# Performance work log

Hardware: AMD Instinct MI355X
Metric: run time of the kernel (lower is better)

The kernel has to match this reference:

```python
import jax, jax.numpy as jnp
import numpy as np

B, N, D_IN, D_OUT, H = 2, 2048, 1024, 1024, 16
HEAD_DIM = D_OUT // H


def setup_inputs() -> dict:
    key = jax.random.key(0)
    ks = jax.random.split(key, 8)
    s = 0.02
    return {
        "x": jax.random.normal(ks[0], (B, N, D_IN), dtype=jnp.float32),
        "Wq": jax.random.normal(ks[1], (D_IN, D_OUT), dtype=jnp.float32) * s,
        "Wk": jax.random.normal(ks[2], (D_IN, D_OUT), dtype=jnp.float32) * s,
        "Wv": jax.random.normal(ks[3], (D_IN, D_OUT), dtype=jnp.float32) * s,
        "Wo": jax.random.normal(ks[4], (D_OUT, D_OUT), dtype=jnp.float32) * s,
        "bo": jnp.zeros((D_OUT,), dtype=jnp.float32),
        "w": jax.random.uniform(ks[5], (H,), dtype=jnp.float32),
        "v": jax.random.uniform(ks[6], (H,), dtype=jnp.float32),
    }


def reference(x, Wq, Wk, Wv, Wo, bo, w, v):
    b, n, _ = x.shape
    h = w.shape[0]
    hd = Wq.shape[1] // h

    # QKV projections -> [b, h, n, hd]
    def proj(W):
        return (x @ W).reshape(b, n, h, hd).transpose(0, 2, 1, 3)

    q, k, val = proj(Wq), proj(Wk), proj(Wv)

    # relative-distance decay R_hat: [h, n, n]
    pos = jnp.arange(n)
    R = jnp.abs(pos[:, None] - pos[None, :]).astype(x.dtype)  # [n, n]
    wv = w[:, None, None]
    vv = v[:, None, None]
    R_hat = (1.0 + jnp.exp(vv)) / (1.0 + jnp.exp(vv - wv * R))  # [h, n, n]

    # ReLU(QK^T) * R_hat, causal mask, scaled softmax
    scores = jax.nn.relu(jnp.einsum("bhqd,bhkd->bhqk", q, k)) * R_hat[None]
    causal = jnp.triu(jnp.ones((n, n), dtype=bool), k=1)
    scores = jnp.where(causal[None, None], -jnp.inf, scores)
    attn = jax.nn.softmax(scores / np.sqrt(hd).astype(x.dtype), axis=-1)

    ctx = jnp.einsum("bhqk,bhkd->bhqd", attn, val)
    ctx = ctx.transpose(0, 2, 1, 3).reshape(b, n, h * hd)
    return ctx @ Wo + bo
```

## Files before the change

kernel.cpp:

```cpp
#include <hip/hip_runtime.h>

typedef unsigned short u16;
typedef unsigned int u32;
typedef __attribute__((ext_vector_type(8))) short bf16x8;
typedef __attribute__((ext_vector_type(4))) float f32x4;

__device__ __forceinline__ u16 f2bf(float f) {
    u32 u = __float_as_uint(f);
    u += 0x7fffu + ((u >> 16) & 1u);
    return (u16)(u >> 16);
}

__device__ __forceinline__ u32 cvtpk(float lo, float hi) {
    u32 r;
    asm("v_cvt_pk_bf16_f32 %0, %1, %2" : "=v"(r) : "v"(lo), "v"(hi));
    return r;
}

#define GL2LDS(gp, lp)                                                                 \
    __builtin_amdgcn_global_load_lds((const __attribute__((address_space(1))) u32*)(const void*)(gp), \
                                     (__attribute__((address_space(3))) u32*)(void*)(lp), 16, 0, 0)

__global__ __launch_bounds__(256) void prep_kernel(const float* __restrict__ x,
                                                   const float* __restrict__ Wq,
                                                   const float* __restrict__ Wk,
                                                   const float* __restrict__ Wv,
                                                   const float* __restrict__ Wo,
                                                   const float* __restrict__ wp,
                                                   const float* __restrict__ vp,
                                                   u16* __restrict__ xb,
                                                   u16* __restrict__ Wcat,
                                                   u16* __restrict__ Wot,
                                                   float* __restrict__ tab,
                                                   u32* __restrict__ counter) {
    __shared__ float tl[32][33];
    const int bid = blockIdx.x, t = threadIdx.x;
    if (bid < 4096) {
        const int i = bid * 256 + t;
        float4 val = ((const float4*)x)[i];
        uint2 o;
        o.x = cvtpk(val.x, val.y);
        o.y = cvtpk(val.z, val.w);
        ((uint2*)xb)[i] = o;
    } else if (bid < 8192) {
        const int tid = bid - 4096;
        const int zi = tid >> 10, rem = tid & 1023;
        const int kt = (rem >> 5) * 32, nt = (rem & 31) * 32;
        const float* src = (zi == 0) ? Wq : (zi == 1) ? Wk : (zi == 2) ? Wv : Wo;
        u16* dst = (zi < 3) ? (Wcat + zi * 1048576) : Wot;
        const int tx = t & 31, ty = t >> 5;
#pragma unroll
        for (int j = 0; j < 4; ++j)
            tl[ty + j * 8][tx] = src[(kt + ty + j * 8) * 1024 + nt + tx];
        __syncthreads();
#pragma unroll
        for (int j = 0; j < 4; ++j)
            dst[(nt + ty + j * 8) * 1024 + kt + tx] = f2bf(tl[tx][ty + j * 8]);
    } else {
        const int i = (bid - 8192) * 256 + t;
        if (i == 0) counter[0] = 0u;
        const int h = i >> 11, d = i & 2047;
        const float vv = vp[h], ww = wp[h];
        tab[i] = (1.f + expf(vv)) / (1.f + expf(vv - ww * (float)d)) *
                 (0.125f * 1.44269504088896340736f);
    }
}

template <int MODE, int BN>
__global__ __launch_bounds__(256, 3) void gemm128(const u16* __restrict__ A,
                                                  const u16* __restrict__ Bt,
                                                  float* __restrict__ C,
                                                  const float* __restrict__ bias,
                                                  u16* __restrict__ Cb,
                                                  u16* __restrict__ Vt,
                                                  int M, int N, int K) {
    constexpr int NBW = BN / 32;
    __shared__ __align__(16) u16 As[8192];
    __shared__ __align__(16) u16 Bs[BN * 64];
    const int t = threadIdx.x, lane = t & 63, wv = t >> 6;
    const int l15 = lane & 15, quad = lane >> 4;
    const int m0 = blockIdx.y << 7, n0 = blockIdx.x * BN;
    const int wm = (wv & 1) << 6, wn = (wv >> 1) * (BN / 2);

    f32x4 acc[4][NBW];
#pragma unroll
    for (int i = 0; i < 4; ++i)
#pragma unroll
        for (int j = 0; j < NBW; ++j) acc[i][j] = (f32x4){0.f, 0.f, 0.f, 0.f};

    const int lrow = lane >> 3, lchunk = lane & 7;
    for (int k0 = 0; k0 < K; k0 += 64) {
#pragma unroll
        for (int c = 0; c < 4; ++c) {
            const int r0 = wv * 32 + c * 8;
            const int row = r0 + lrow;
            const int g = lchunk ^ (row & 7);
            GL2LDS(A + (size_t)(m0 + row) * K + k0 + g * 8, &As[r0 * 64]);
        }
#pragma unroll
        for (int c = 0; c < BN / 32; ++c) {
            const int r0 = wv * (BN / 4) + c * 8;
            const int row = r0 + lrow;
            const int g = lchunk ^ (row & 7);
            GL2LDS(Bt + (size_t)(n0 + row) * K + k0 + g * 8, &Bs[r0 * 64]);
        }
        __syncthreads();
#pragma unroll
        for (int ks = 0; ks < 2; ++ks) {
            const int p = ((ks << 2) | quad) ^ (l15 & 7);
            bf16x8 af[4], bfr[NBW];
#pragma unroll
            for (int i = 0; i < 4; ++i)
                af[i] = *(const bf16x8*)&As[(wm + i * 16 + l15) * 64 + p * 8];
#pragma unroll
            for (int j = 0; j < NBW; ++j)
                bfr[j] = *(const bf16x8*)&Bs[(wn + j * 16 + l15) * 64 + p * 8];
#pragma unroll
            for (int mb = 0; mb < 4; ++mb)
#pragma unroll
                for (int nb = 0; nb < NBW; ++nb)
                    acc[mb][nb] = __builtin_amdgcn_mfma_f32_16x16x32_bf16(af[mb], bfr[nb],
                                                                          acc[mb][nb], 0, 0, 0);
        }
        __syncthreads();
    }
    const int rb = m0 + wm + (quad << 2);
    const int cbase = n0 + wn + l15;
#pragma unroll
    for (int mb = 0; mb < 4; ++mb)
#pragma unroll
        for (int nb = 0; nb < NBW; ++nb) {
            const int col = cbase + nb * 16;
            if (MODE == 0) {
#pragma unroll
                for (int r = 0; r < 4; ++r) {
                    const int row = rb + mb * 16 + r;
                    C[(size_t)row * N + col] = acc[mb][nb][r] + bias[col];
                }
            } else if (col < 2048) {
#pragma unroll
                for (int r = 0; r < 4; ++r) {
                    const int row = rb + mb * 16 + r;
                    Cb[(size_t)row * 2048 + col] = f2bf(acc[mb][nb][r]);
                }
            } else {
                const int pos = (((mb >> 1) * 4 + quad) << 3) + ((mb & 1) << 2);
                uint2 o;
                o.x = cvtpk(acc[mb][nb][0], acc[mb][nb][1]);
                o.y = cvtpk(acc[mb][nb][2], acc[mb][nb][3]);
                *(uint2*)(Vt + (size_t)(col - 2048) * 4096 + (m0 + wm) + pos) = o;
            }
        }
}

__global__ __launch_bounds__(256, 3) void attn_kernel(const u16* __restrict__ qkb,
                                                      const u16* __restrict__ vtb,
                                                      const float* __restrict__ rtab,
                                                      u16* __restrict__ ctxb,
                                                      u32* __restrict__ counter) {
    __shared__ __align__(16) u16 Kt[2][4096];
    __shared__ __align__(16) u16 Vt2[2][4096];
    __shared__ __align__(16) float rall[2048];
    __shared__ int jobS;

    const int t = threadIdx.x, lane = t & 63, wv = t >> 6;
    const int l15 = lane & 15, quad = lane >> 4;
    const int lrow = lane >> 3, lchunk = lane & 7;
    const int half0 = (wv & 1) * 32;

    for (;;) {
        if (t == 0) jobS = (int)atomicAdd(counter, 1u);
        __syncthreads();
        const int job = jobS;
        if (job >= 1024) break;
        const int qt = 31 - (job >> 5);
        const int bh = job & 31;
        const int b = bh >> 4, h = bh & 15;
        const int q0 = qt << 6;

        {
            const float4* src = (const float4*)(rtab + (h << 11));
            const int nf = (q0 + 64) >> 2;
            for (int i = t; i < nf; i += 256) ((float4*)rall)[i] = src[i];
        }

        bf16x8 qb[2];
        {
            const u16* qrow = qkb + (size_t)(b * 2048 + q0 + (wv << 4) + l15) * 2048 +
                              (h << 6) + quad * 8;
            qb[0] = *(const bf16x8*)(qrow);
            qb[1] = *(const bf16x8*)(qrow + 32);
        }

        f32x4 cacc[4];
#pragma unroll
        for (int i = 0; i < 4; ++i) cacc[i] = (f32x4){0.f, 0.f, 0.f, 0.f};
        f32x4 lacc4 = (f32x4){0.f, 0.f, 0.f, 0.f};

#pragma unroll
        for (int c = 0; c < 4; ++c) {
            const int r0 = half0 + c * 8;
            const int row = r0 + lrow;
            const int g = lchunk ^ (row & 7);
            if (wv < 2)
                GL2LDS(qkb + (size_t)(b * 2048 + row) * 2048 + 1024 + (h << 6) + g * 8,
                       &Kt[0][r0 * 64]);
            else
                GL2LDS(vtb + (size_t)((h << 6) + row) * 4096 + b * 2048 + g * 8,
                       &Vt2[0][r0 * 64]);
        }

        for (int kt = 0; kt <= qt; ++kt) {
            const int bsel = kt & 1;
            __syncthreads();
            if (kt < qt) {
                const int kg0 = (kt + 1) << 6;
#pragma unroll
                for (int c = 0; c < 4; ++c) {
                    const int r0 = half0 + c * 8;
                    const int row = r0 + lrow;
                    const int g = lchunk ^ (row & 7);
                    if (wv < 2)
                        GL2LDS(qkb + (size_t)(b * 2048 + kg0 + row) * 2048 + 1024 + (h << 6) + g * 8,
                               &Kt[bsel ^ 1][r0 * 64]);
                    else
                        GL2LDS(vtb + (size_t)((h << 6) + row) * 4096 + b * 2048 + kg0 + g * 8,
                               &Vt2[bsel ^ 1][r0 * 64]);
                }
            }

            f32x4 sacc[4];
#pragma unroll
            for (int i = 0; i < 4; ++i) sacc[i] = (f32x4){0.f, 0.f, 0.f, 0.f};
            __builtin_amdgcn_s_setprio(1);
#pragma unroll
            for (int ks = 0; ks < 2; ++ks) {
                const int p = ((ks << 2) | quad) ^ (l15 & 7);
#pragma unroll
                for (int mb = 0; mb < 4; ++mb) {
                    bf16x8 ka = *(const bf16x8*)&Kt[bsel][(mb * 16 + l15) * 64 + p * 8];
                    sacc[mb] = __builtin_amdgcn_mfma_f32_16x16x32_bf16(ka, qb[ks],
                                                                       sacc[mb], 0, 0, 0);
                }
            }
            __builtin_amdgcn_s_setprio(0);

            const int D0 = q0 - (kt << 6) + (wv << 4) + l15;
            u32 pk[4][2];
            if (kt < qt) {
#pragma unroll
                for (int mb = 0; mb < 4; ++mb) {
                    float pe[4];
#pragma unroll
                    for (int r = 0; r < 4; ++r) {
                        const int dist = D0 - (mb * 16 + (quad << 2) + r);
                        pe[r] = exp2f(fmaxf(sacc[mb][r], 0.f) * rall[dist]);
                        lacc4[r] += pe[r];
                    }
                    pk[mb][0] = cvtpk(pe[0], pe[1]);
                    pk[mb][1] = cvtpk(pe[2], pe[3]);
                }
            } else {
#pragma unroll
                for (int mb = 0; mb < 4; ++mb) {
                    float pe[4];
#pragma unroll
                    for (int r = 0; r < 4; ++r) {
                        const int dist = D0 - (mb * 16 + (quad << 2) + r);
                        const int di = dist < 0 ? 0 : dist;
                        float p0 = exp2f(fmaxf(sacc[mb][r], 0.f) * rall[di]);
                        pe[r] = (dist < 0) ? 0.f : p0;
                        lacc4[r] += pe[r];
                    }
                    pk[mb][0] = cvtpk(pe[0], pe[1]);
                    pk[mb][1] = cvtpk(pe[2], pe[3]);
                }
            }

            __builtin_amdgcn_s_setprio(1);
#pragma unroll
            for (int ks = 0; ks < 2; ++ks) {
                int4 pv = {(int)pk[2 * ks][0], (int)pk[2 * ks][1],
                           (int)pk[2 * ks + 1][0], (int)pk[2 * ks + 1][1]};
                bf16x8 pb = *(bf16x8*)&pv;
                const int g = (4 * ks + quad) ^ (l15 & 7);
#pragma unroll
                for (int db = 0; db < 4; ++db) {
                    bf16x8 vf = *(const bf16x8*)&Vt2[bsel][(db * 16 + l15) * 64 + g * 8];
                    cacc[db] = __builtin_amdgcn_mfma_f32_16x16x32_bf16(vf, pb,
                                                                       cacc[db], 0, 0, 0);
                }
            }
            __builtin_amdgcn_s_setprio(0);
        }

        float lt = (lacc4[0] + lacc4[1]) + (lacc4[2] + lacc4[3]);
        lt += __shfl_xor(lt, 16, 64);
        lt += __shfl_xor(lt, 32, 64);
        const float inv = 1.f / lt;
        u16* op = ctxb + (size_t)(b * 2048 + q0 + (wv << 4) + l15) * 1024 +
                  (h << 6) + (quad << 2);
#pragma unroll
        for (int db = 0; db < 4; ++db) {
            uint2 o;
            o.x = cvtpk(cacc[db][0] * inv, cacc[db][1] * inv);
            o.y = cvtpk(cacc[db][2] * inv, cacc[db][3] * inv);
            *(uint2*)(op + db * 16) = o;
        }
    }
}

extern "C" void kernel_launch(void* const* d_in, const int* in_sizes, int n_in,
                              void* d_out, int out_size, void* d_ws, size_t ws_size,
                              hipStream_t stream) {
    const float* x  = (const float*)d_in[0];
    const float* Wq = (const float*)d_in[1];
    const float* Wk = (const float*)d_in[2];
    const float* Wv = (const float*)d_in[3];
    const float* Wo = (const float*)d_in[4];
    const float* bo = (const float*)d_in[5];
    const float* w  = (const float*)d_in[6];
    const float* v  = (const float*)d_in[7];
    float* out = (float*)d_out;

    char* w8 = (char*)d_ws;
    u16*  xb   = (u16*)(w8);
    u16*  Wcat = (u16*)(w8 + (8u << 20));
    u16*  Wot  = (u16*)(w8 + (14u << 20));
    u16*  qkb  = (u16*)(w8 + (16u << 20));
    u16*  vtb  = (u16*)(w8 + (32u << 20));
    u16*  ctxb = (u16*)(w8 + (40u << 20));
    float* rtab = (float*)(w8 + (48u << 20));
    u32*  counter = (u32*)(w8 + (48u << 20) + (1u << 17));

    prep_kernel<<<8320, 256, 0, stream>>>(x, Wq, Wk, Wv, Wo, w, v, xb, Wcat, Wot, rtab,
                                          counter);
    gemm128<1, 128><<<dim3(24, 32), 256, 0, stream>>>(xb, Wcat, nullptr, nullptr, qkb, vtb,
                                                      4096, 3072, 1024);
    attn_kernel<<<768, 256, 0, stream>>>(qkb, vtb, rtab, ctxb, counter);
    gemm128<0, 64><<<dim3(16, 32), 256, 0, stream>>>(ctxb, Wot, out, bo, nullptr, nullptr,
                                                     4096, 1024, 1024);
}
```

Measured before the change: 186.0 us.

## Triple-buffer K tiles and split K/V barriers with explicit vmcnt waits

Restructures the attention inner loop so K tiles are prefetched two iterations ahead into a triple buffer while V stays double-buffered. Each iteration now has two barriers: one before QK^T and another before PV. Explicit s_waitcnt vmcnt counts replace the compiler's conservative waits, so the V load can land during the softmax work. This adds LDS usage, which may reduce occupancy at the 3-blocks-per-CU bound, and adds an extra barrier per tile.

```diff
diff --git a/kernel.cpp b/kernel.cpp
--- a/kernel.cpp
+++ b/kernel.cpp
@@ -20,6 +20,18 @@
 #define GL2LDS(gp, lp)                                                                 \
     __builtin_amdgcn_global_load_lds((const __attribute__((address_space(1))) u32*)(const void*)(gp), \
                                      (__attribute__((address_space(3))) u32*)(void*)(lp), 16, 0, 0)
+
+#define SBAR                                                                           \
+    do {                                                                               \
+        __builtin_amdgcn_sched_barrier(0);                                             \
+        __builtin_amdgcn_s_barrier();                                                  \
+        __builtin_amdgcn_sched_barrier(0);                                             \
+    } while (0)
+#define WAITV(N)                                                                       \
+    do {                                                                               \
+        asm volatile("s_waitcnt vmcnt(" #N ")" ::: "memory");                          \
+        __builtin_amdgcn_sched_barrier(0);                                             \
+    } while (0)
 
 __global__ __launch_bounds__(256) void prep_kernel(const float* __restrict__ x,
                                                    const float* __restrict__ Wq,
@@ -158,7 +170,7 @@
                                                       const float* __restrict__ rtab,
                                                       u16* __restrict__ ctxb,
                                                       u32* __restrict__ counter) {
-    __shared__ __align__(16) u16 Kt[2][4096];
+    __shared__ __align__(16) u16 Kt[3][4096];
     __shared__ __align__(16) u16 Vt2[2][4096];
     __shared__ __align__(16) float rall[2048];
     __shared__ int jobS;
@@ -192,41 +204,54 @@
             qb[1] = *(const bf16x8*)(qrow + 32);
         }
 
+        auto stage_k = [&](int ktile, int kb) {
+#pragma unroll
+            for (int c = 0; c < 4; ++c) {
+                const int r0 = half0 + c * 8;
+                const int row = r0 + lrow;
+                const int g = lchunk ^ (row & 7);
+                GL2LDS(qkb + (size_t)(b * 2048 + (ktile << 6) + row) * 2048 + 1024 +
+                           (h << 6) + g * 8,
+                       &Kt[kb][r0 * 64]);
+            }
+        };
+        auto stage_v = [&](int ktile, int vb) {
+#pragma unroll
+            for (int c = 0; c < 4; ++c) {
+                const int r0 = half0 + c * 8;
+                const int row = r0 + lrow;
+                const int g = lchunk ^ (row & 7);
+                GL2LDS(vtb + (size_t)((h << 6) + row) * 4096 + b * 2048 + (ktile << 6) +
+                           g * 8,
+                       &Vt2[vb][r0 * 64]);
+            }
+        };
+
         f32x4 cacc[4];
 #pragma unroll
         for (int i = 0; i < 4; ++i) cacc[i] = (f32x4){0.f, 0.f, 0.f, 0.f};
         f32x4 lacc4 = (f32x4){0.f, 0.f, 0.f, 0.f};
 
-#pragma unroll
-        for (int c = 0; c < 4; ++c) {
-            const int r0 = half0 + c * 8;
-            const int row = r0 + lrow;
-            const int g = lchunk ^ (row & 7);
-            if (wv < 2)
-                GL2LDS(qkb + (size_t)(b * 2048 + row) * 2048 + 1024 + (h << 6) + g * 8,
-                       &Kt[0][r0 * 64]);
-            else
-                GL2LDS(vtb + (size_t)((h << 6) + row) * 4096 + b * 2048 + g * 8,
-                       &Vt2[0][r0 * 64]);
-        }
+        if (wv < 2) {
+            stage_k(0, 0);
+            if (qt >= 1) stage_k(1, 1);
+        } else {
+            stage_v(0, 0);
+        }
+        asm volatile("s_waitcnt lgkmcnt(0)" ::: "memory");
+        __builtin_amdgcn_sched_barrier(0);
 
         for (int kt = 0; kt <= qt; ++kt) {
-            const int bsel = kt & 1;
-            __syncthreads();
-            if (kt < qt) {
-                const int kg0 = (kt + 1) << 6;
-#pragma unroll
-                for (int c = 0; c < 4; ++c) {
-                    const int r0 = half0 + c * 8;
-                    const int row = r0 + lrow;
-                    const int g = lchunk ^ (row & 7);
-                    if (wv < 2)
-                        GL2LDS(qkb + (size_t)(b * 2048 + kg0 + row) * 2048 + 1024 + (h << 6) + g * 8,
-                               &Kt[bsel ^ 1][r0 * 64]);
-                    else
-                        GL2LDS(vtb + (size_t)((h << 6) + row) * 4096 + b * 2048 + kg0 + g * 8,
-                               &Vt2[bsel ^ 1][r0 * 64]);
-                }
+            const int kb = kt % 3, vb = kt & 1;
+            if (wv < 2) {
+                if (kt < qt) WAITV(4);
+                else         WAITV(0);
+            }
+            SBAR;
+            if (wv < 2) {
+                if (kt + 2 <= qt) stage_k(kt + 2, (kt + 2) % 3);
+            } else {
+                if (kt + 1 <= qt) stage_v(kt + 1, (kt + 1) & 1);
             }
 
             f32x4 sacc[4];
@@ -238,7 +263,7 @@
                 const int p = ((ks << 2) | quad) ^ (l15 & 7);
 #pragma unroll
                 for (int mb = 0; mb < 4; ++mb) {
-                    bf16x8 ka = *(const bf16x8*)&Kt[bsel][(mb * 16 + l15) * 64 + p * 8];
+                    bf16x8 ka = *(const bf16x8*)&Kt[kb][(mb * 16 + l15) * 64 + p * 8];
                     sacc[mb] = __builtin_amdgcn_mfma_f32_16x16x32_bf16(ka, qb[ks],
                                                                        sacc[mb], 0, 0, 0);
                 }
@@ -277,6 +302,12 @@
                 }
             }
 
+            if (wv >= 2) {
+                if (kt < qt) WAITV(4);
+                else         WAITV(0);
+            }
+            SBAR;
+
             __builtin_amdgcn_s_setprio(1);
 #pragma unroll
             for (int ks = 0; ks < 2; ++ks) {
@@ -286,7 +317,7 @@
                 const int g = (4 * ks + quad) ^ (l15 & 7);
 #pragma unroll
                 for (int db = 0; db < 4; ++db) {
-                    bf16x8 vf = *(const bf16x8*)&Vt2[bsel][(db * 16 + l15) * 64 + g * 8];
+                    bf16x8 vf = *(const bf16x8*)&Vt2[vb][(db * 16 + l15) * 64 + g * 8];
                     cacc[db] = __builtin_amdgcn_mfma_f32_16x16x32_bf16(vf, pb,
                                                                        cacc[db], 0, 0, 0);
                 }
```

New measurement: 184.3 us. About the same (-0.9%).
